# Performance work log

Measured on AMD Instinct MI355X. Metric: run time of the kernel, lower is better.

## Reference

```python
import jax, jax.numpy as jnp
import numpy as np

B, N, D, C, NCLS = 8, 2048, 256, 128, 50
EPS = 1e-5  # BatchNorm eps

def _bn(x, g, b):
    # eval-mode BatchNorm1d over channel dim of (B,C,N): running_mean=0, running_var=1
    return x * (g / jnp.sqrt(1.0 + EPS))[:, None] + b[:, None]

def _complex_linear(x, Wr, br, Wi, bi):
    # torch ComplexLinear: complex(fr(x.real)-fi(x.imag), fr(x.imag)+fi(x.real))
    xr, xi = x.real, x.imag
    re = (xr @ Wr.T + br) - (xi @ Wi.T + bi)
    im = (xi @ Wr.T + br) + (xr @ Wi.T + bi)
    return jax.lax.complex(re, im)

def _sa(x, qkW, vW, vb, tW, tb, g, b):
    # x: (B,C,N); q/k share weights (tied in torch), dim C//4
    xq = jnp.einsum('qc,bcn->bnq', qkW, x)            # (B,N,C/4)
    xk = jnp.einsum('qc,bcm->bqm', qkW, x)            # (B,C/4,N)
    energy = jnp.einsum('bnq,bqm->bnm', xq, xk)       # (B,N,N)
    attn = jax.nn.softmax(energy, axis=-1)
    attn = attn / (1e-9 + attn.sum(axis=1, keepdims=True))  # column renorm
    xv = jnp.einsum('oc,bcn->bon', vW, x) + vb[:, None]
    xr = x - jnp.einsum('bcn,bnm->bcm', xv, attn)
    xr = jnp.einsum('oc,bcn->bon', tW, xr) + tb[:, None]
    return x + jax.nn.relu(_bn(xr, g, b))

def reference(xyz, cls_label, A, Bmat, W1r, b1r, W1i, b1i, W2r, b2r, W2i, b2i,
              lbl_emb, ft_w1, ft_g1, ft_b1, ft_w2, ft_g2, ft_b2,
              sa_qk, sa_vw, sa_vb, sa_tw, sa_tb, sa_g, sa_b,
              fuse_w, fuse_g, fuse_b, c1_w, c1_b, bn1_g, bn1_b, c2_w, c2_b):
    pts = xyz.transpose(0, 2, 1)                       # (B,N,3)
    # VecKM(d=256, alpha=30, beta=9): G = eB (eB^H eA), normalized to sqrt(d)
    eA = jnp.exp(1j * (pts @ A))                       # (B,N,D) complex64
    eB = jnp.exp(1j * (pts @ Bmat))
    inner = jnp.einsum('bnd,bne->bde', eB.conj(), eA)  # (B,D,D)
    G = jnp.einsum('bnd,bde->bne', eB, inner)          # (B,N,D)
    G = G / jnp.linalg.norm(G, axis=-1, keepdims=True) * jnp.sqrt(jnp.float32(D))
    G = _complex_linear(G, W1r, b1r, W1i, b1i)
    G = jax.lax.complex(jax.nn.relu(G.real), jax.nn.relu(G.imag))  # ComplexReLU
    G = _complex_linear(G, W2r, b2r, W2i, b2i)
    G = (G.real ** 2 + G.imag ** 2).transpose(0, 2, 1)  # (B,D,N)
    reweight = (cls_label @ lbl_emb)[:, :, None]        # (B,D,1)
    x = G * reweight
    x = jax.nn.relu(_bn(jnp.einsum('oc,bcn->bon', ft_w1, x), ft_g1, ft_b1))
    x = _bn(jnp.einsum('oc,bcn->bon', ft_w2, x), ft_g2, ft_b2)  # (B,C,N)
    feats = []
    for i in range(4):
        x = _sa(x, sa_qk[i], sa_vw[i], sa_vb[i], sa_tw[i], sa_tb[i], sa_g[i], sa_b[i])
        feats.append(x)
    x = jnp.concatenate(feats, axis=1)                  # (B,4C,N)
    x = jax.nn.relu(_bn(jnp.einsum('oc,bcn->bon', fuse_w, x), fuse_g, fuse_b))
    x = jax.nn.relu(_bn(jnp.einsum('oc,bcn->bon', c1_w, x) + c1_b[:, None], bn1_g, bn1_b))
    # dropout is identity in eval mode
    x = jnp.einsum('oc,bcn->bon', c2_w, x) + c2_b[:, None]
    x = jax.nn.log_softmax(x, axis=1)
    return x.transpose(0, 2, 1)                         # (B,N,NCLS)

def setup_inputs():
    key = jax.random.key(0)
    k = jax.random.split(key, 24)
    rn = lambda i, s: jax.random.normal(k[i], s, jnp.float32)
    s = 0.05
    return {
        'xyz': rn(0, (B, 3, N)),
        'cls_label': jax.random.uniform(k[1], (B, 16), jnp.float32),
        'A': rn(2, (3, D)) * 30.0,
        'Bmat': rn(3, (3, D)) * 9.0,
        'W1r': rn(4, (D, D)) * s, 'b1r': rn(5, (D,)) * s,
        'W1i': rn(6, (D, D)) * s, 'b1i': rn(7, (D,)) * s,
        'W2r': rn(8, (D, D)) * s, 'b2r': rn(9, (D,)) * s,
        'W2i': rn(10, (D, D)) * s, 'b2i': rn(11, (D,)) * s,
        'lbl_emb': rn(12, (16, D)),
        'ft_w1': rn(13, (C, D)) * s, 'ft_g1': jnp.ones((C,)), 'ft_b1': jnp.zeros((C,)),
        'ft_w2': rn(14, (C, C)) * s, 'ft_g2': jnp.ones((C,)), 'ft_b2': jnp.zeros((C,)),
        'sa_qk': rn(15, (4, C // 4, C)) * s,
        'sa_vw': rn(16, (4, C, C)) * s, 'sa_vb': rn(17, (4, C)) * s,
        'sa_tw': rn(18, (4, C, C)) * s, 'sa_tb': rn(19, (4, C)) * s,
        'sa_g': jnp.ones((4, C)), 'sa_b': jnp.zeros((4, C)),
        'fuse_w': rn(20, (C, 4 * C)) * s, 'fuse_g': jnp.ones((C,)), 'fuse_b': jnp.zeros((C,)),
        'c1_w': rn(21, (C, C)) * s, 'c1_b': rn(22, (C,)) * s,
        'bn1_g': jnp.ones((C,)), 'bn1_b': jnp.zeros((C,)),
        'c2_w': rn(23, (NCLS, C)) * s, 'c2_b': jnp.zeros((NCLS,)),
    }
```

## Files before the change

### kernel.cpp

```cpp
#include <hip/hip_runtime.h>

#define BB 8
#define NPTS 2048
#define DD 256
#define CCH 128
#define NCLASS 50
#define LOG2E 1.4426950408889634f

typedef __attribute__((ext_vector_type(8))) short short8;
typedef __attribute__((ext_vector_type(4))) float f32x4;
typedef unsigned short u16;
#define MFMA16(a,b,c) __builtin_amdgcn_mfma_f32_16x16x32_bf16(a,b,c,0,0,0)

__device__ __forceinline__ u16 f2bf(float x){
  union { float f; unsigned int u; } v; v.f = x;
  unsigned int r = v.u + 0x7FFFu + ((v.u >> 16) & 1u);
  return (u16)(r >> 16);
}
__device__ __forceinline__ float bf2f(u16 u){
  union { unsigned int u32; float f; } v; v.u32 = ((unsigned int)u) << 16; return v.f;
}
__device__ __forceinline__ void split2(float x, u16& h, u16& l){
  h = f2bf(x); l = f2bf(x - bf2f(h));
}
__device__ __forceinline__ short8 ld8(const u16* p){ return *(const short8*)p; }
__device__ __forceinline__ short8 zero8(){ short8 z = {0,0,0,0,0,0,0,0}; return z; }

struct WSplit {
  const float* src[12];
  int cnt[12];
  int off[12];
};
__global__ __launch_bounds__(256) void wsplit_kernel(WSplit wsp, u16* __restrict__ H,
                                                     u16* __restrict__ L)
{
  int seg = blockIdx.y;
  int idx = blockIdx.x*256 + threadIdx.x;
  if (idx >= wsp.cnt[seg]) return;
  float v = wsp.src[seg][idx];
  u16 h, l; split2(v, h, l);
  H[wsp.off[seg]+idx] = h; L[wsp.off[seg]+idx] = l;
}

__global__ __launch_bounds__(256) void ek1_kernel(
    const float* __restrict__ xyz, const float* __restrict__ A, const float* __restrict__ Bm,
    u16* __restrict__ ATrh, u16* __restrict__ ATrl, u16* __restrict__ ATih, u16* __restrict__ ATil,
    u16* __restrict__ BTrh, u16* __restrict__ BTrl, u16* __restrict__ BTih, u16* __restrict__ BTil)
{
  size_t idx = (size_t)blockIdx.x*256 + threadIdx.x;
  int n = (int)(idx & (NPTS-1));
  int d = (int)((idx >> 11) & (DD-1));
  int b = (int)(idx >> 19);
  float p0 = xyz[((size_t)b*3+0)*NPTS+n];
  float p1 = xyz[((size_t)b*3+1)*NPTS+n];
  float p2 = xyz[((size_t)b*3+2)*NPTS+n];
  float phA = p0*A[d] + p1*A[DD+d] + p2*A[2*DD+d];
  float phB = p0*Bm[d] + p1*Bm[DD+d] + p2*Bm[2*DD+d];
  float sa, ca, sb, cb;
  sincosf(phA, &sa, &ca);
  sincosf(phB, &sb, &cb);
  size_t off = ((size_t)b*DD + d)*NPTS + n;
  u16 h, l;
  split2(ca, h, l); ATrh[off] = h; ATrl[off] = l;
  split2(sa, h, l); ATih[off] = h; ATil[off] = l;
  split2(cb, h, l); BTrh[off] = h; BTrl[off] = l;
  split2(sb, h, l); BTih[off] = h; BTil[off] = l;
}

__global__ __launch_bounds__(256) void ek2_kernel(
    const float* __restrict__ xyz, const float* __restrict__ Bm,
    u16* __restrict__ Brh, u16* __restrict__ Brl, u16* __restrict__ Bih, u16* __restrict__ Bil)
{
  size_t idx = (size_t)blockIdx.x*256 + threadIdx.x;
  int d = (int)(idx & (DD-1));
  int n = (int)((idx >> 8) & (NPTS-1));
  int b = (int)(idx >> 19);
  float p0 = xyz[((size_t)b*3+0)*NPTS+n];
  float p1 = xyz[((size_t)b*3+1)*NPTS+n];
  float p2 = xyz[((size_t)b*3+2)*NPTS+n];
  float phB = p0*Bm[d] + p1*Bm[DD+d] + p2*Bm[2*DD+d];
  float sb, cb;
  sincosf(phB, &sb, &cb);
  size_t off = ((size_t)b*NPTS + n)*DD + d;
  u16 h, l;
  split2(cb, h, l); Brh[off] = h; Brl[off] = l;
  split2(sb, h, l); Bih[off] = h; Bil[off] = l;
}

__global__ __launch_bounds__(256) void inner_mfma_kernel(
    const u16* __restrict__ ATrh, const u16* __restrict__ ATrl,
    const u16* __restrict__ ATih, const u16* __restrict__ ATil,
    const u16* __restrict__ BTrh, const u16* __restrict__ BTrl,
    const u16* __restrict__ BTih, const u16* __restrict__ BTil,
    float2* __restrict__ PART)
{
  int z = blockIdx.z; int b = z & 7; int ch = z >> 3;
  int e0 = blockIdx.y*64, d0 = blockIdx.x*64;
  int tid = threadIdx.x, lane = tid & 63, w = tid >> 6;
  int wr = (w >> 1)*32, wc = (w & 1)*32;
  int r16 = lane & 15, g4 = lane >> 4;
  f32x4 re[2][2] = {}, ip[2][2] = {}, iq[2][2] = {};
  size_t ar_[2], br_[2];
  #pragma unroll
  for (int rg = 0; rg < 2; rg++) {
    ar_[rg] = ((size_t)b*DD + (e0 + wr + rg*16 + r16))*NPTS + g4*8;
    br_[rg] = ((size_t)b*DD + (d0 + wc + rg*16 + r16))*NPTS + g4*8;
  }
  int kbeg = ch*512;
  #pragma unroll 2
  for (int kk = 0; kk < 512; kk += 32) {
    int k0 = kbeg + kk;
    short8 arh[2], arl[2], aih[2], ail[2], brh[2], brl[2], bih[2], bil[2];
    #pragma unroll
    for (int rg = 0; rg < 2; rg++) {
      arh[rg] = ld8(ATrh + ar_[rg] + k0); arl[rg] = ld8(ATrl + ar_[rg] + k0);
      aih[rg] = ld8(ATih + ar_[rg] + k0); ail[rg] = ld8(ATil + ar_[rg] + k0);
      brh[rg] = ld8(BTrh + br_[rg] + k0); brl[rg] = ld8(BTrl + br_[rg] + k0);
      bih[rg] = ld8(BTih + br_[rg] + k0); bil[rg] = ld8(BTil + br_[rg] + k0);
    }
    #pragma unroll
    for (int ra = 0; ra < 2; ra++)
      #pragma unroll
      for (int rb = 0; rb < 2; rb++) {
        re[ra][rb] = MFMA16(arh[ra], brh[rb], re[ra][rb]);
        re[ra][rb] = MFMA16(arh[ra], brl[rb], re[ra][rb]);
        re[ra][rb] = MFMA16(arl[ra], brh[rb], re[ra][rb]);
        re[ra][rb] = MFMA16(aih[ra], bih[rb], re[ra][rb]);
        re[ra][rb] = MFMA16(aih[ra], bil[rb], re[ra][rb]);
        re[ra][rb] = MFMA16(ail[ra], bih[rb], re[ra][rb]);
        ip[ra][rb] = MFMA16(aih[ra], brh[rb], ip[ra][rb]);
        ip[ra][rb] = MFMA16(aih[ra], brl[rb], ip[ra][rb]);
        ip[ra][rb] = MFMA16(ail[ra], brh[rb], ip[ra][rb]);
        iq[ra][rb] = MFMA16(arh[ra], bih[rb], iq[ra][rb]);
        iq[ra][rb] = MFMA16(arh[ra], bil[rb], iq[ra][rb]);
        iq[ra][rb] = MFMA16(arl[ra], bih[rb], iq[ra][rb]);
      }
  }
  float2* outp = PART + ((size_t)(ch*BB + b)*DD)*DD;
  #pragma unroll
  for (int ra = 0; ra < 2; ra++)
    #pragma unroll
    for (int rb = 0; rb < 2; rb++)
      #pragma unroll
      for (int j = 0; j < 4; j++) {
        int e = e0 + wr + ra*16 + g4*4 + j;
        int d = d0 + wc + rb*16 + r16;
        outp[(size_t)e*DD + d] = make_float2(re[ra][rb][j], ip[ra][rb][j] - iq[ra][rb][j]);
      }
}

__global__ __launch_bounds__(256) void innred_kernel(const float2* __restrict__ P,
    u16* __restrict__ Irh, u16* __restrict__ Irl, u16* __restrict__ Iih, u16* __restrict__ Iil)
{
  size_t i = (size_t)blockIdx.x*256 + threadIdx.x;
  const size_t S = (size_t)BB*DD*DD;
  float2 a = P[i], b = P[i+S], c = P[i+2*S], d = P[i+3*S];
  float rr = a.x+b.x+c.x+d.x, ii = a.y+b.y+c.y+d.y;
  u16 h, l;
  split2(rr, h, l); Irh[i] = h; Irl[i] = l;
  split2(ii, h, l); Iih[i] = h; Iil[i] = l;
}

__global__ __launch_bounds__(256) void g_mfma_kernel(
    const u16* __restrict__ Brh, const u16* __restrict__ Brl,
    const u16* __restrict__ Bih, const u16* __restrict__ Bil,
    const u16* __restrict__ Irh, const u16* __restrict__ Irl,
    const u16* __restrict__ Iih, const u16* __restrict__ Iil,
    float2* __restrict__ G)
{
  int b = blockIdx.z;
  int n0 = blockIdx.y*64, e0 = blockIdx.x*64;
  int tid = threadIdx.x, lane = tid & 63, w = tid >> 6;
  int wr = (w >> 1)*32, wc = (w & 1)*32;
  int r16 = lane & 15, g4 = lane >> 4;
  f32x4 p[2][2] = {}, q[2][2] = {}, im[2][2] = {};
  size_t ar_[2], br_[2];
  #pragma unroll
  for (int rg = 0; rg < 2; rg++) {
    ar_[rg] = ((size_t)b*NPTS + (n0 + wr + rg*16 + r16))*DD + g4*8;
    br_[rg] = ((size_t)b*DD + (e0 + wc + rg*16 + r16))*DD + g4*8;
  }
  #pragma unroll
  for (int k0 = 0; k0 < DD; k0 += 32) {
    short8 arh[2], arl[2], aih[2], ail[2], brh[2], brl[2], bih[2], bil[2];
    #pragma unroll
    for (int rg = 0; rg < 2; rg++) {
      arh[rg] = ld8(Brh + ar_[rg] + k0); arl[rg] = ld8(Brl + ar_[rg] + k0);
      aih[rg] = ld8(Bih + ar_[rg] + k0); ail[rg] = ld8(Bil + ar_[rg] + k0);
      brh[rg] = ld8(Irh + br_[rg] + k0); brl[rg] = ld8(Irl + br_[rg] + k0);
      bih[rg] = ld8(Iih + br_[rg] + k0); bil[rg] = ld8(Iil + br_[rg] + k0);
    }
    #pragma unroll
    for (int ra = 0; ra < 2; ra++)
      #pragma unroll
      for (int rb = 0; rb < 2; rb++) {
        p[ra][rb] = MFMA16(arh[ra], brh[rb], p[ra][rb]);
        p[ra][rb] = MFMA16(arh[ra], brl[rb], p[ra][rb]);
        p[ra][rb] = MFMA16(arl[ra], brh[rb], p[ra][rb]);
        q[ra][rb] = MFMA16(aih[ra], bih[rb], q[ra][rb]);
        q[ra][rb] = MFMA16(aih[ra], bil[rb], q[ra][rb]);
        q[ra][rb] = MFMA16(ail[ra], bih[rb], q[ra][rb]);
        im[ra][rb] = MFMA16(arh[ra], bih[rb], im[ra][rb]);
        im[ra][rb] = MFMA16(arh[ra], bil[rb], im[ra][rb]);
        im[ra][rb] = MFMA16(arl[ra], bih[rb], im[ra][rb]);
        im[ra][rb] = MFMA16(aih[ra], brh[rb], im[ra][rb]);
        im[ra][rb] = MFMA16(aih[ra], brl[rb], im[ra][rb]);
        im[ra][rb] = MFMA16(ail[ra], brh[rb], im[ra][rb]);
      }
  }
  #pragma unroll
  for (int ra = 0; ra < 2; ra++)
    #pragma unroll
    for (int rb = 0; rb < 2; rb++)
      #pragma unroll
      for (int j = 0; j < 4; j++) {
        int n = n0 + wr + ra*16 + g4*4 + j;
        int e = e0 + wc + rb*16 + r16;
        G[((size_t)b*NPTS + n)*DD + e] = make_float2(p[ra][rb][j] - q[ra][rb][j], im[ra][rb][j]);
      }
}

__global__ __launch_bounds__(256) void gnormsplit_kernel(const float2* __restrict__ Gf,
    u16* __restrict__ Grh, u16* __restrict__ Grl, u16* __restrict__ Gih, u16* __restrict__ Gil)
{
  size_t row = blockIdx.x;
  const float2* p = Gf + row*DD;
  int tid = threadIdx.x;
  float2 v = p[tid];
  __shared__ float red[256];
  red[tid] = v.x*v.x + v.y*v.y;
  __syncthreads();
  for (int w = 128; w > 0; w >>= 1) { if (tid < w) red[tid] += red[tid+w]; __syncthreads(); }
  float sc = 16.f * rsqrtf(red[0]);
  size_t off = row*DD + tid;
  u16 h, l;
  split2(v.x*sc, h, l); Grh[off] = h; Grl[off] = l;
  split2(v.y*sc, h, l); Gih[off] = h; Gil[off] = l;
}

__global__ __launch_bounds__(256) void clinear_mfma_kernel(
    const u16* __restrict__ Arh, const u16* __restrict__ Arl,
    const u16* __restrict__ Aih, const u16* __restrict__ Ail,
    const u16* __restrict__ Wrh, const u16* __restrict__ Wrl,
    const u16* __restrict__ Wih, const u16* __restrict__ Wil,
    const float* __restrict__ br, const float* __restrict__ bi,
    u16* __restrict__ Orh, u16* __restrict__ Orl, u16* __restrict__ Oih, u16* __restrict__ Oil,
    const float* __restrict__ RW, float* __restrict__ GSQ, int mode)
{
  int wg = blockIdx.y * gridDim.x + blockIdx.x;
  int xcd = wg & 7, idx = wg >> 3;
  int o0 = (idx & 3) * 64;
  int m0 = (xcd * ((int)gridDim.y >> 3) + (idx >> 2)) * 64;
  int tid = threadIdx.x, lane = tid & 63, w = tid >> 6;
  int wr = (w >> 1)*32, wc = (w & 1)*32;
  int r16 = lane & 15, g4 = lane >> 4;
  f32x4 p[2][2] = {}, q[2][2] = {}, im[2][2] = {};
  size_t ar_[2], br_[2];
  #pragma unroll
  for (int rg = 0; rg < 2; rg++) {
    ar_[rg] = (size_t)(m0 + wr + rg*16 + r16)*DD + g4*8;
    br_[rg] = (size_t)(o0 + wc + rg*16 + r16)*DD + g4*8;
  }
  #pragma unroll
  for (int k0 = 0; k0 < DD; k0 += 32) {
    short8 arh[2], arl[2], aih[2], ail[2], brh[2], brl[2], bih[2], bil[2];
    #pragma unroll
    for (int rg = 0; rg < 2; rg++) {
      arh[rg] = ld8(Arh + ar_[rg] + k0); arl[rg] = ld8(Arl + ar_[rg] + k0);
      aih[rg] = ld8(Aih + ar_[rg] + k0); ail[rg] = ld8(Ail + ar_[rg] + k0);
      brh[rg] = ld8(Wrh + br_[rg] + k0); brl[rg] = ld8(Wrl + br_[rg] + k0);
      bih[rg] = ld8(Wih + br_[rg] + k0); bil[rg] = ld8(Wil + br_[rg] + k0);
    }
    #pragma unroll
    for (int ra = 0; ra < 2; ra++)
      #pragma unroll
      for (int rb = 0; rb < 2; rb++) {
        p[ra][rb] = MFMA16(arh[ra], brh[rb], p[ra][rb]);
        p[ra][rb] = MFMA16(arh[ra], brl[rb], p[ra][rb]);
        p[ra][rb] = MFMA16(arl[ra], brh[rb], p[ra][rb]);
        q[ra][rb] = MFMA16(aih[ra], bih[rb], q[ra][rb]);
        q[ra][rb] = MFMA16(aih[ra], bil[rb], q[ra][rb]);
        q[ra][rb] = MFMA16(ail[ra], bih[rb], q[ra][rb]);
        im[ra][rb] = MFMA16(arh[ra], bih[rb], im[ra][rb]);
        im[ra][rb] = MFMA16(arh[ra], bil[rb], im[ra][rb]);
        im[ra][rb] = MFMA16(arl[ra], bih[rb], im[ra][rb]);
        im[ra][rb] = MFMA16(aih[ra], brh[rb], im[ra][rb]);
        im[ra][rb] = MFMA16(aih[ra], brl[rb], im[ra][rb]);
        im[ra][rb] = MFMA16(ail[ra], brh[rb], im[ra][rb]);
      }
  }
  #pragma unroll
  for (int ra = 0; ra < 2; ra++)
    #pragma unroll
    for (int rb = 0; rb < 2; rb++) {
      int o = o0 + wc + rb*16 + r16;
      float brv = br[o], biv = bi[o];
      if (mode == 1) {
        #pragma unroll
        for (int j = 0; j < 4; j++) {
          int m = m0 + wr + ra*16 + g4*4 + j;
          float re = fmaxf(p[ra][rb][j] - q[ra][rb][j] + brv - biv, 0.f);
          float iv = fmaxf(im[ra][rb][j] + brv + biv, 0.f);
          size_t off = (size_t)m*DD + o;
          u16 h, l;
          split2(re, h, l); Orh[off] = h; Orl[off] = l;
          split2(iv, h, l); Oih[off] = h; Oil[off] = l;
        }
      } else {
        int mbase = m0 + wr + ra*16 + g4*4;
        int b = mbase >> 11, nb = mbase & (NPTS-1);
        float rwv = RW[(size_t)b*DD + o];
        float4 gv;
        #pragma unroll
        for (int j = 0; j < 4; j++) {
          float re = p[ra][rb][j] - q[ra][rb][j] + brv - biv;
          float iv = im[ra][rb][j] + brv + biv;
          ((float*)&gv)[j] = (re*re + iv*iv) * rwv;
        }
        *(float4*)(GSQ + ((size_t)b*DD + o)*NPTS + nb) = gv;
      }
    }
}

__global__ void rw_kernel(const float* __restrict__ cls, const float* __restrict__ lbl,
                          float* __restrict__ RW)
{
  int b = blockIdx.x; int d = threadIdx.x;
  float s = 0.f;
  #pragma unroll
  for (int k = 0; k < 16; k++) s += cls[b*16+k] * lbl[k*DD+d];
  RW[b*DD+d] = s;
}

__global__ __launch_bounds__(256) void sgemm_kernel(
    const u16* __restrict__ Wh, const u16* __restrict__ Wl,
    const float* __restrict__ X, float* __restrict__ Y,
    const float* __restrict__ RES,
    const float* __restrict__ bias, const float* __restrict__ bng, const float* __restrict__ bnb,
    u16* __restrict__ YBh, u16* __restrict__ YBl, int ybmode,
    int O, int Cin, size_t xbs, size_t ybs, size_t rbs, int flags)
{
  int b = blockIdx.z;
  int n0 = blockIdx.x*64, o0 = blockIdx.y*64;
  const float* x = X + (size_t)b*xbs;
  __shared__ u16 sXh[64][40], sXl[64][40];
  int tid = threadIdx.x, lane = tid & 63, w = tid >> 6;
  int wo = (w >> 1)*32, wn = (w & 1)*32;
  int r16 = lane & 15, g4 = lane >> 4;
  f32x4 acc[2][2] = {};
  int stc = tid >> 3;
  int stn = (tid & 7)*8;
  for (int k0 = 0; k0 < Cin; k0 += 32) {
    const float* px = x + (size_t)(k0+stc)*NPTS + n0 + stn;
    float4 u0 = *(const float4*)px;
    float4 u1 = *(const float4*)(px+4);
    float v[8] = {u0.x,u0.y,u0.z,u0.w,u1.x,u1.y,u1.z,u1.w};
    __syncthreads();
    #pragma unroll
    for (int j = 0; j < 8; j++) {
      u16 h, l; split2(v[j], h, l);
      sXh[stn+j][stc] = h; sXl[stn+j][stc] = l;
    }
    __syncthreads();
    short8 awh[2], awl[2], bxh[2], bxl[2];
    #pragma unroll
    for (int rg = 0; rg < 2; rg++) {
      int orow = o0 + wo + rg*16 + r16;
      if (orow < O) {
        size_t woff = (size_t)orow*Cin + k0 + g4*8;
        awh[rg] = ld8(Wh + woff); awl[rg] = ld8(Wl + woff);
      } else { awh[rg] = zero8(); awl[rg] = zero8(); }
      bxh[rg] = ld8(&sXh[wn + rg*16 + r16][g4*8]);
      bxl[rg] = ld8(&sXl[wn + rg*16 + r16][g4*8]);
    }
    #pragma unroll
    for (int ra = 0; ra < 2; ra++)
      #pragma unroll
      for (int rb = 0; rb < 2; rb++) {
        acc[ra][rb] = MFMA16(awh[ra], bxh[rb], acc[ra][rb]);
        acc[ra][rb] = MFMA16(awh[ra], bxl[rb], acc[ra][rb]);
        acc[ra][rb] = MFMA16(awl[ra], bxh[rb], acc[ra][rb]);
      }
  }
  #pragma unroll
  for (int ra = 0; ra < 2; ra++)
    #pragma unroll
    for (int rb = 0; rb < 2; rb++)
      #pragma unroll
      for (int j = 0; j < 4; j++) {
        int o = o0 + wo + ra*16 + g4*4 + j;
        if (o >= O) continue;
        int n = n0 + wn + rb*16 + r16;
        float v = acc[ra][rb][j];
        if (flags & 1) v += bias[o];
        if (flags & 2) v = v * (bng[o] * rsqrtf(1.f + 1e-5f)) + bnb[o];
        if (flags & 4) v = fmaxf(v, 0.f);
        if (flags & 8) v += RES[(size_t)b*rbs + (size_t)o*NPTS + n];
        if (ybmode == 0) Y[(size_t)b*ybs + (size_t)o*NPTS + n] = v;
        else if (ybmode == 1) YBh[(size_t)b*ybs + (size_t)o*NPTS + n] = f2bf(v);
        else {
          u16 h, l; split2(v, h, l);
          size_t off = ((size_t)b*NPTS + n)*32 + o;
          YBh[off] = h; YBl[off] = l;
        }
      }
}

__global__ __launch_bounds__(256) void sastat_kernel(
    const u16* __restrict__ Qh, const u16* __restrict__ Ql,
    float* __restrict__ PM, float* __restrict__ PS)
{
  int b = blockIdx.z, ch = blockIdx.y;
  int n0 = blockIdx.x*64;
  size_t base = (size_t)b*NPTS*32;
  int tid = threadIdx.x, lane = tid & 63, wid = tid >> 6;
  int r16 = lane & 15, g4 = lane >> 4;
  size_t ao = base + (size_t)(n0 + wid*16 + r16)*32 + g4*8;
  short8 ah = ld8(Qh + ao), al = ld8(Ql + ao);
  float pm[4] = {-3.4e38f,-3.4e38f,-3.4e38f,-3.4e38f};
  float ps[4] = {0.f,0.f,0.f,0.f};
  int mbeg = ch*512, mend = mbeg + 512;
  for (int mt = mbeg; mt < mend; mt += 32) {
    size_t bo0 = base + (size_t)(mt + r16)*32 + g4*8;
    size_t bo1 = bo0 + 16*32;
    short8 bh0 = ld8(Qh+bo0), bl0 = ld8(Ql+bo0);
    short8 bh1 = ld8(Qh+bo1), bl1 = ld8(Ql+bo1);
    f32x4 a0 = {}, a1 = {};
    a0 = MFMA16(ah, bh0, a0); a0 = MFMA16(ah, bl0, a0); a0 = MFMA16(al, bh0, a0);
    a1 = MFMA16(ah, bh1, a1); a1 = MFMA16(ah, bl1, a1); a1 = MFMA16(al, bh1, a1);
    #pragma unroll
    for (int j = 0; j < 4; j++) {
      float v = fmaxf(a0[j], a1[j]);
      float mn = fmaxf(pm[j], v);
      ps[j] = ps[j]*exp2f((pm[j]-mn)*LOG2E)
            + exp2f((a0[j]-mn)*LOG2E) + exp2f((a1[j]-mn)*LOG2E);
      pm[j] = mn;
    }
  }
  #pragma unroll
  for (int j = 0; j < 4; j++) {
    float m = pm[j], s = ps[j];
    #pragma unroll
    for (int d = 1; d < 16; d <<= 1) {
      float om = __shfl_xor(m, d);
      float os = __shfl_xor(s, d);
      float mn = fmaxf(m, om);
      s = s*exp2f((m-mn)*LOG2E) + os*exp2f((om-mn)*LOG2E);
      m = mn;
    }
    if (r16 == 0) {
      int n_ = n0 + wid*16 + g4*4 + j;
      size_t off = ((size_t)ch*BB + b)*NPTS + n_;
      PM[off] = m; PS[off] = s;
    }
  }
}

__global__ __launch_bounds__(256) void comb1_kernel(
    const float* __restrict__ PM, const float* __restrict__ PS,
    float* __restrict__ MX, float* __restrict__ RS)
{
  size_t i = (size_t)blockIdx.x*256 + threadIdx.x;
  const size_t S = (size_t)BB*NPTS;
  float m0 = PM[i], m1 = PM[i+S], m2 = PM[i+2*S], m3 = PM[i+3*S];
  float mx = fmaxf(fmaxf(m0,m1), fmaxf(m2,m3));
  float den = PS[i]*exp2f((m0-mx)*LOG2E) + PS[i+S]*exp2f((m1-mx)*LOG2E)
            + PS[i+2*S]*exp2f((m2-mx)*LOG2E) + PS[i+3*S]*exp2f((m3-mx)*LOG2E);
  MX[i] = mx; RS[i] = 1.f/den;
}

__global__ __launch_bounds__(512) void fused_pv_kernel(
    const u16* __restrict__ Qh, const u16* __restrict__ Ql,
    const float* __restrict__ MX, const float* __restrict__ RS,
    const u16* __restrict__ XV, const float* __restrict__ XRES, size_t res_bs,
    float* __restrict__ OUT)
{
  int b = blockIdx.y;
  int m0 = blockIdx.x*64;
  size_t qbase = (size_t)b*NPTS*32;
  const u16* xv = XV + (size_t)b*CCH*NPTS;
  __shared__ float smx[NPTS], srs[NPTS];
  __shared__ u16 Pl[64][36];
  __shared__ float csacc[64];
  int tid = threadIdx.x, lane = tid & 63, w = tid >> 6;
  int r16 = lane & 15, g4 = lane >> 4;
  for (int t = tid; t < NPTS; t += 512) {
    smx[t] = MX[(size_t)b*NPTS + t];
    srs[t] = RS[(size_t)b*NPTS + t];
  }
  if (tid < 64) csacc[tid] = 0.f;
  int ma = w >> 1, na = w & 1;
  int cw = (w >> 1)*32, mw = (w & 1)*32;
  size_t eao = qbase + (size_t)(m0 + ma*16 + r16)*32 + g4*8;
  short8 eah = ld8(Qh + eao), eal = ld8(Ql + eao);
  const u16* pa0 = xv + (size_t)(cw + r16)*NPTS + g4*8;
  const u16* pa1 = pa0 + (size_t)16*NPTS;
  f32x4 acc[2][2] = {};
  float cs[4] = {0.f,0.f,0.f,0.f};
  size_t ebo = qbase + (size_t)(na*16 + r16)*32 + g4*8;
  short8 ebh = ld8(Qh + ebo), ebl = ld8(Ql + ebo);
  short8 xa0 = ld8(pa0), xa1 = ld8(pa1);
  __syncthreads();
  for (int nt = 0; nt < NPTS; nt += 32) {
    f32x4 e = {};
    e = MFMA16(eah, ebh, e); e = MFMA16(eah, ebl, e); e = MFMA16(eal, ebh, e);
    int nn = nt + na*16 + r16;
    float mxv_ = smx[nn], rsv_ = srs[nn];
    #pragma unroll
    for (int j = 0; j < 4; j++) {
      float t = exp2f((e[j]-mxv_)*LOG2E)*rsv_;
      cs[j] += t;
      Pl[ma*16 + g4*4 + j][na*16 + r16] = f2bf(t);
    }
    short8 nebh = zero8(), nebl = zero8(), nxa0 = zero8(), nxa1 = zero8();
    if (nt + 32 < NPTS) {
      size_t ebo2 = qbase + (size_t)(nt + 32 + na*16 + r16)*32 + g4*8;
      nebh = ld8(Qh + ebo2); nebl = ld8(Ql + ebo2);
      nxa0 = ld8(pa0 + nt + 32); nxa1 = ld8(pa1 + nt + 32);
    }
    __syncthreads();
    short8 b0 = *(const short8*)&Pl[mw + r16][g4*8];
    short8 b1 = *(const short8*)&Pl[mw + 16 + r16][g4*8];
    acc[0][0] = MFMA16(xa0, b0, acc[0][0]);
    acc[0][1] = MFMA16(xa0, b1, acc[0][1]);
    acc[1][0] = MFMA16(xa1, b0, acc[1][0]);
    acc[1][1] = MFMA16(xa1, b1, acc[1][1]);
    __syncthreads();
    ebh = nebh; ebl = nebl; xa0 = nxa0; xa1 = nxa1;
  }
  #pragma unroll
  for (int j = 0; j < 4; j++) {
    float c = cs[j];
    #pragma unroll
    for (int d = 1; d < 16; d <<= 1) c += __shfl_xor(c, d);
    if (r16 == 0) atomicAdd(&csacc[ma*16 + g4*4 + j], c);
  }
  __syncthreads();
  #pragma unroll
  for (int ca = 0; ca < 2; ca++)
    #pragma unroll
    for (int mb = 0; mb < 2; mb++) {
      int m = m0 + mw + mb*16 + r16;
      float ci = 1.f/(1e-9f + csacc[mw + mb*16 + r16]);
      #pragma unroll
      for (int j = 0; j < 4; j++) {
        int c = cw + ca*16 + g4*4 + j;
        float v = XRES[(size_t)b*res_bs + (size_t)c*NPTS + m] - acc[ca][mb][j]*ci;
        OUT[((size_t)b*CCH + c)*NPTS + m] = v;
      }
    }
}

__global__ __launch_bounds__(256) void lsm_kernel(const float* __restrict__ Y,
                                                  float* __restrict__ OUT)
{
  int idx = blockIdx.x*256 + threadIdx.x;
  int b = idx >> 11, n = idx & (NPTS-1);
  const float* p = Y + (size_t)b*NCLASS*NPTS + n;
  float m = -3.4e38f;
  #pragma unroll
  for (int k = 0; k < NCLASS; k++) m = fmaxf(m, p[(size_t)k*NPTS]);
  float s = 0.f;
  #pragma unroll
  for (int k = 0; k < NCLASS; k++) s += expf(p[(size_t)k*NPTS] - m);
  float L = m + logf(s);
  float* o = OUT + (size_t)idx*NCLASS;
  #pragma unroll
  for (int k = 0; k < NCLASS; k++) o[k] = p[(size_t)k*NPTS] - L;
}

extern "C" void kernel_launch(void* const* d_in, const int* in_sizes, int n_in,
                              void* d_out, int out_size, void* d_ws, size_t ws_size,
                              hipStream_t stream)
{
  (void)in_sizes; (void)n_in; (void)out_size; (void)ws_size;
  const float* xyz  = (const float*)d_in[0];
  const float* cls  = (const float*)d_in[1];
  const float* Amat = (const float*)d_in[2];
  const float* Bm   = (const float*)d_in[3];
  const float* W1r  = (const float*)d_in[4];
  const float* b1r  = (const float*)d_in[5];
  const float* W1i  = (const float*)d_in[6];
  const float* b1i  = (const float*)d_in[7];
  const float* W2r  = (const float*)d_in[8];
  const float* b2r  = (const float*)d_in[9];
  const float* W2i  = (const float*)d_in[10];
  const float* b2i  = (const float*)d_in[11];
  const float* lbl  = (const float*)d_in[12];
  const float* ftw1 = (const float*)d_in[13];
  const float* ftg1 = (const float*)d_in[14];
  const float* ftb1 = (const float*)d_in[15];
  const float* ftw2 = (const float*)d_in[16];
  const float* ftg2 = (const float*)d_in[17];
  const float* ftb2 = (const float*)d_in[18];
  const float* saqk = (const float*)d_in[19];
  const float* savw = (const float*)d_in[20];
  const float* savb = (const float*)d_in[21];
  const float* satw = (const float*)d_in[22];
  const float* satb = (const float*)d_in[23];
  const float* sag  = (const float*)d_in[24];
  const float* sab  = (const float*)d_in[25];
  const float* fusew= (const float*)d_in[26];
  const float* fuseg= (const float*)d_in[27];
  const float* fuseb= (const float*)d_in[28];
  const float* c1w  = (const float*)d_in[29];
  const float* c1b  = (const float*)d_in[30];
  const float* bn1g = (const float*)d_in[31];
  const float* bn1b = (const float*)d_in[32];
  const float* c2w  = (const float*)d_in[33];
  const float* c2b  = (const float*)d_in[34];
  float* out = (float*)d_out;

  float* ws = (float*)d_ws;
  const size_t PS  = (size_t)BB*DD*NPTS;
  const size_t ISZ = (size_t)BB*DD*DD;
  u16* U = (u16*)ws;
  u16 *ATrh = U+0*PS, *ATrl = U+1*PS, *ATih = U+2*PS, *ATil = U+3*PS;
  u16 *BTrh = U+4*PS, *BTrl = U+5*PS, *BTih = U+6*PS, *BTil = U+7*PS;
  u16 *Bnrh = U+8*PS, *Bnrl = U+9*PS, *Bnih = U+10*PS, *Bnil = U+11*PS;
  u16 *Irh = U+12*PS, *Irl = U+12*PS+ISZ, *Iih = U+12*PS+2*ISZ, *Iil = U+12*PS+3*ISZ;
  float* gsq = (float*)(U + 12*PS + 4*ISZ);
  float2* PART = (float2*)gsq;
  float2* Gf = (float2*)ws;
  u16 *G1rh = U+4*PS, *G1rl = U+5*PS, *G1ih = U+6*PS, *G1il = U+7*PS;
  u16 *G2rh = U+8*PS, *G2rl = U+9*PS, *G2ih = U+10*PS, *G2il = U+11*PS;
  size_t p = (size_t)BB*NPTS*NPTS;
  float* xfeat = ws + p;  p += (size_t)BB*CCH*NPTS;
  float* feats = ws + p;  p += (size_t)BB*4*CCH*NPTS;
  float* xt1   = ws + p;  p += (size_t)BB*CCH*NPTS;
  float* xt2   = ws + p;  p += (size_t)BB*CCH*NPTS;
  float* ybuf  = ws + p;  p += (size_t)BB*NCLASS*NPTS;
  float* rwb   = ws + p;  p += (size_t)BB*DD;
  float* mxv   = ws + p;  p += (size_t)BB*NPTS;
  float* rsv   = ws + p;  p += (size_t)BB*NPTS;
  float* PMb   = ws + p;  p += (size_t)4*BB*NPTS;
  float* PSb   = ws + p;  p += (size_t)4*BB*NPTS;
  u16* xqh = (u16*)(ws + p);
  u16* xql = xqh + (size_t)BB*NPTS*32;
  u16* xvb = xql + (size_t)BB*NPTS*32;
  u16* wpH = xvb + (size_t)BB*CCH*NPTS;
  u16* wpL = wpH + 557056;

  const int o_w1r=0, o_w1i=65536, o_w2r=131072, o_w2i=196608, o_ft1=262144,
            o_ft2=294912, o_qk=311296, o_vw=327680, o_tw=393216, o_fu=458752,
            o_c1=524288, o_c2=540672;
  WSplit wsp;
  const float* srcs[12] = {W1r,W1i,W2r,W2i,ftw1,ftw2,saqk,savw,satw,fusew,c1w,c2w};
  const int cnts[12] = {65536,65536,65536,65536,32768,16384,16384,65536,65536,65536,16384,6400};
  const int offs[12] = {o_w1r,o_w1i,o_w2r,o_w2i,o_ft1,o_ft2,o_qk,o_vw,o_tw,o_fu,o_c1,o_c2};
  for (int i = 0; i < 12; i++) { wsp.src[i]=srcs[i]; wsp.cnt[i]=cnts[i]; wsp.off[i]=offs[i]; }

  wsplit_kernel<<<dim3(256, 12), 256, 0, stream>>>(wsp, wpH, wpL);
  rw_kernel<<<BB, DD, 0, stream>>>(cls, lbl, rwb);
  ek1_kernel<<<(int)(PS/256), 256, 0, stream>>>(xyz, Amat, Bm,
      ATrh, ATrl, ATih, ATil, BTrh, BTrl, BTih, BTil);
  ek2_kernel<<<(int)(PS/256), 256, 0, stream>>>(xyz, Bm, Bnrh, Bnrl, Bnih, Bnil);
  inner_mfma_kernel<<<dim3(DD/64, DD/64, BB*4), 256, 0, stream>>>(
      ATrh, ATrl, ATih, ATil, BTrh, BTrl, BTih, BTil, PART);
  innred_kernel<<<(int)(ISZ/256), 256, 0, stream>>>(PART, Irh, Irl, Iih, Iil);
  g_mfma_kernel<<<dim3(DD/64, NPTS/64, BB), 256, 0, stream>>>(
      Bnrh, Bnrl, Bnih, Bnil, Irh, Irl, Iih, Iil, Gf);
  gnormsplit_kernel<<<BB*NPTS, 256, 0, stream>>>(Gf, G1rh, G1rl, G1ih, G1il);
  clinear_mfma_kernel<<<dim3(DD/64, (BB*NPTS)/64), 256, 0, stream>>>(
      G1rh, G1rl, G1ih, G1il, wpH+o_w1r, wpL+o_w1r, wpH+o_w1i, wpL+o_w1i,
      b1r, b1i, G2rh, G2rl, G2ih, G2il, nullptr, nullptr, 1);
  clinear_mfma_kernel<<<dim3(DD/64, (BB*NPTS)/64), 256, 0, stream>>>(
      G2rh, G2rl, G2ih, G2il, wpH+o_w2r, wpL+o_w2r, wpH+o_w2i, wpL+o_w2i,
      b2r, b2i, nullptr, nullptr, nullptr, nullptr, rwb, gsq, 2);

  sgemm_kernel<<<dim3(NPTS/64, CCH/64, BB), 256, 0, stream>>>(
      wpH+o_ft1, wpL+o_ft1, gsq, xt1, nullptr, nullptr, ftg1, ftb1, nullptr, nullptr, 0,
      CCH, DD, (size_t)DD*NPTS, (size_t)CCH*NPTS, 0, 2|4);
  sgemm_kernel<<<dim3(NPTS/64, CCH/64, BB), 256, 0, stream>>>(
      wpH+o_ft2, wpL+o_ft2, xt1, xfeat, nullptr, nullptr, ftg2, ftb2, nullptr, nullptr, 0,
      CCH, CCH, (size_t)CCH*NPTS, (size_t)CCH*NPTS, 0, 2);

  const float* xsrc = xfeat;
  size_t xbs = (size_t)CCH*NPTS;
  for (int i = 0; i < 4; i++) {
    sgemm_kernel<<<dim3(NPTS/64, 1, BB), 256, 0, stream>>>(
        wpH+o_qk + i*32*CCH, wpL+o_qk + i*32*CCH, xsrc, nullptr, nullptr,
        nullptr, nullptr, nullptr, xqh, xql, 2, 32, CCH, xbs, 0, 0, 0);
    sastat_kernel<<<dim3(NPTS/64, 4, BB), 256, 0, stream>>>(xqh, xql, PMb, PSb);
    comb1_kernel<<<(BB*NPTS)/256, 256, 0, stream>>>(PMb, PSb, mxv, rsv);
    sgemm_kernel<<<dim3(NPTS/64, CCH/64, BB), 256, 0, stream>>>(
        wpH+o_vw + i*CCH*CCH, wpL+o_vw + i*CCH*CCH, xsrc, nullptr, nullptr,
        savb + i*CCH, nullptr, nullptr, xvb, nullptr, 1, CCH, CCH, xbs,
        (size_t)CCH*NPTS, 0, 1);
    fused_pv_kernel<<<dim3(NPTS/64, BB), 512, 0, stream>>>(
        xqh, xql, mxv, rsv, xvb, xsrc, xbs, xt2);
    sgemm_kernel<<<dim3(NPTS/64, CCH/64, BB), 256, 0, stream>>>(
        wpH+o_tw + i*CCH*CCH, wpL+o_tw + i*CCH*CCH, xt2, feats + (size_t)i*CCH*NPTS, xsrc,
        satb + i*CCH, sag + i*CCH, sab + i*CCH, nullptr, nullptr, 0,
        CCH, CCH, (size_t)CCH*NPTS, (size_t)4*CCH*NPTS, xbs, 1|2|4|8);
    xsrc = feats + (size_t)i*CCH*NPTS;
    xbs = (size_t)4*CCH*NPTS;
  }

  sgemm_kernel<<<dim3(NPTS/64, CCH/64, BB), 256, 0, stream>>>(
      wpH+o_fu, wpL+o_fu, feats, xt1, nullptr, nullptr, fuseg, fuseb, nullptr, nullptr, 0,
      CCH, 4*CCH, (size_t)4*CCH*NPTS, (size_t)CCH*NPTS, 0, 2|4);
  sgemm_kernel<<<dim3(NPTS/64, CCH/64, BB), 256, 0, stream>>>(
      wpH+o_c1, wpL+o_c1, xt1, xt2, nullptr, c1b, bn1g, bn1b, nullptr, nullptr, 0,
      CCH, CCH, (size_t)CCH*NPTS, (size_t)CCH*NPTS, 0, 1|2|4);
  sgemm_kernel<<<dim3(NPTS/64, 1, BB), 256, 0, stream>>>(
      wpH+o_c2, wpL+o_c2, xt2, ybuf, nullptr, c2b, nullptr, nullptr, nullptr, nullptr, 0,
      NCLASS, CCH, (size_t)CCH*NPTS, (size_t)NCLASS*NPTS, 0, 1);
  lsm_kernel<<<(BB*NPTS)/256, 256, 0, stream>>>(ybuf, out);
}
```

Baseline: 970.5 us.

## Restructure fused attention-PV kernel to 16-column tiles with double-buffered P

Rewrites the fused softmax-times-V kernel so each 256-thread block handles 16 output columns instead of 64. Each wave computes a 16x16 chunk of attention probabilities for 64 keys per iteration into a double-buffered LDS tile, so one barrier per step is needed instead of two. Row max and inverse sum are read straight from global memory as float4 instead of being staged in LDS. The grid grows fourfold, which raises occupancy but recomputes more energy tiles per value load. The clinear kernel also drops its XCD-aware block swizzle in favour of a plain blockIdx mapping.

```diff
diff --git a/kernel.cpp b/kernel.cpp
--- a/kernel.cpp
+++ b/kernel.cpp
@@ -247,10 +247,7 @@
     u16* __restrict__ Orh, u16* __restrict__ Orl, u16* __restrict__ Oih, u16* __restrict__ Oil,
     const float* __restrict__ RW, float* __restrict__ GSQ, int mode)
 {
-  int wg = blockIdx.y * gridDim.x + blockIdx.x;
-  int xcd = wg & 7, idx = wg >> 3;
-  int o0 = (idx & 3) * 64;
-  int m0 = (xcd * ((int)gridDim.y >> 3) + (idx >> 2)) * 64;
+  int m0 = blockIdx.y*64, o0 = blockIdx.x*64;
   int tid = threadIdx.x, lane = tid & 63, w = tid >> 6;
   int wr = (w >> 1)*32, wc = (w & 1)*32;
   int r16 = lane & 15, g4 = lane >> 4;
@@ -469,85 +466,83 @@
   MX[i] = mx; RS[i] = 1.f/den;
 }
 
-__global__ __launch_bounds__(512) void fused_pv_kernel(
+__global__ __launch_bounds__(256) void fused_pv_kernel(
     const u16* __restrict__ Qh, const u16* __restrict__ Ql,
     const float* __restrict__ MX, const float* __restrict__ RS,
     const u16* __restrict__ XV, const float* __restrict__ XRES, size_t res_bs,
     float* __restrict__ OUT)
 {
   int b = blockIdx.y;
-  int m0 = blockIdx.x*64;
+  int m0 = blockIdx.x*16;
   size_t qbase = (size_t)b*NPTS*32;
   const u16* xv = XV + (size_t)b*CCH*NPTS;
-  __shared__ float smx[NPTS], srs[NPTS];
-  __shared__ u16 Pl[64][36];
-  __shared__ float csacc[64];
+  const float* mx = MX + (size_t)b*NPTS;
+  const float* rs = RS + (size_t)b*NPTS;
+  __shared__ u16 Pl[2][16][72];
+  __shared__ float csacc[16];
   int tid = threadIdx.x, lane = tid & 63, w = tid >> 6;
   int r16 = lane & 15, g4 = lane >> 4;
-  for (int t = tid; t < NPTS; t += 512) {
-    smx[t] = MX[(size_t)b*NPTS + t];
-    srs[t] = RS[(size_t)b*NPTS + t];
-  }
-  if (tid < 64) csacc[tid] = 0.f;
-  int ma = w >> 1, na = w & 1;
-  int cw = (w >> 1)*32, mw = (w & 1)*32;
-  size_t eao = qbase + (size_t)(m0 + ma*16 + r16)*32 + g4*8;
-  short8 eah = ld8(Qh + eao), eal = ld8(Ql + eao);
+  if (tid < 16) csacc[tid] = 0.f;
+  int nb = w;
+  int cw = w*32;
+  int nloc = nb*16 + g4*4;
+  size_t mo = qbase + (size_t)(m0 + r16)*32 + g4*8;
+  short8 mbh = ld8(Qh + mo), mbl = ld8(Ql + mo);
   const u16* pa0 = xv + (size_t)(cw + r16)*NPTS + g4*8;
   const u16* pa1 = pa0 + (size_t)16*NPTS;
-  f32x4 acc[2][2] = {};
-  float cs[4] = {0.f,0.f,0.f,0.f};
-  size_t ebo = qbase + (size_t)(na*16 + r16)*32 + g4*8;
-  short8 ebh = ld8(Qh + ebo), ebl = ld8(Ql + ebo);
-  short8 xa0 = ld8(pa0), xa1 = ld8(pa1);
+  f32x4 acc[2] = {};
+  float csl = 0.f;
+
+  #define COMPUTE_P(NT, BUF) { \
+    size_t no_ = qbase + (size_t)((NT) + nb*16 + r16)*32 + g4*8; \
+    short8 nah = ld8(Qh + no_), nal = ld8(Ql + no_); \
+    f32x4 e = {}; \
+    e = MFMA16(nah, mbh, e); e = MFMA16(nah, mbl, e); e = MFMA16(nal, mbh, e); \
+    float4 mx4 = *(const float4*)&mx[(NT) + nloc]; \
+    float4 rs4 = *(const float4*)&rs[(NT) + nloc]; \
+    float t0 = exp2f((e[0]-mx4.x)*LOG2E)*rs4.x; \
+    float t1 = exp2f((e[1]-mx4.y)*LOG2E)*rs4.y; \
+    float t2 = exp2f((e[2]-mx4.z)*LOG2E)*rs4.z; \
+    float t3 = exp2f((e[3]-mx4.w)*LOG2E)*rs4.w; \
+    csl += t0 + t1 + t2 + t3; \
+    uint2 pk; \
+    pk.x = (unsigned)f2bf(t0) | ((unsigned)f2bf(t1) << 16); \
+    pk.y = (unsigned)f2bf(t2) | ((unsigned)f2bf(t3) << 16); \
+    *(uint2*)&Pl[BUF][r16][nloc] = pk; }
+
+  COMPUTE_P(0, 0);
   __syncthreads();
-  for (int nt = 0; nt < NPTS; nt += 32) {
-    f32x4 e = {};
-    e = MFMA16(eah, ebh, e); e = MFMA16(eah, ebl, e); e = MFMA16(eal, ebh, e);
-    int nn = nt + na*16 + r16;
-    float mxv_ = smx[nn], rsv_ = srs[nn];
+  int cur = 0;
+  for (int nt = 0; nt < NPTS; nt += 64) {
+    short8 xa0 = ld8(pa0 + nt), xa1 = ld8(pa1 + nt);
+    short8 xb0 = ld8(pa0 + nt + 32), xb1 = ld8(pa1 + nt + 32);
+    short8 p0  = *(const short8*)&Pl[cur][r16][g4*8];
+    short8 p0b = *(const short8*)&Pl[cur][r16][32 + g4*8];
+    if (nt + 64 < NPTS) { COMPUTE_P(nt + 64, cur ^ 1); }
+    acc[0] = MFMA16(xa0, p0, acc[0]);
+    acc[1] = MFMA16(xa1, p0, acc[1]);
+    acc[0] = MFMA16(xb0, p0b, acc[0]);
+    acc[1] = MFMA16(xb1, p0b, acc[1]);
+    __syncthreads();
+    cur ^= 1;
+  }
+  #undef COMPUTE_P
+  {
+    float c = csl;
+    c += __shfl_xor(c, 16);
+    c += __shfl_xor(c, 32);
+    if (g4 == 0) atomicAdd(&csacc[r16], c);
+  }
+  __syncthreads();
+  float ci = 1.f/(1e-9f + csacc[r16]);
+  int m = m0 + r16;
+  #pragma unroll
+  for (int ca = 0; ca < 2; ca++)
     #pragma unroll
     for (int j = 0; j < 4; j++) {
-      float t = exp2f((e[j]-mxv_)*LOG2E)*rsv_;
-      cs[j] += t;
-      Pl[ma*16 + g4*4 + j][na*16 + r16] = f2bf(t);
-    }
-    short8 nebh = zero8(), nebl = zero8(), nxa0 = zero8(), nxa1 = zero8();
-    if (nt + 32 < NPTS) {
-      size_t ebo2 = qbase + (size_t)(nt + 32 + na*16 + r16)*32 + g4*8;
-      nebh = ld8(Qh + ebo2); nebl = ld8(Ql + ebo2);
-      nxa0 = ld8(pa0 + nt + 32); nxa1 = ld8(pa1 + nt + 32);
-    }
-    __syncthreads();
-    short8 b0 = *(const short8*)&Pl[mw + r16][g4*8];
-    short8 b1 = *(const short8*)&Pl[mw + 16 + r16][g4*8];
-    acc[0][0] = MFMA16(xa0, b0, acc[0][0]);
-    acc[0][1] = MFMA16(xa0, b1, acc[0][1]);
-    acc[1][0] = MFMA16(xa1, b0, acc[1][0]);
-    acc[1][1] = MFMA16(xa1, b1, acc[1][1]);
-    __syncthreads();
-    ebh = nebh; ebl = nebl; xa0 = nxa0; xa1 = nxa1;
-  }
-  #pragma unroll
-  for (int j = 0; j < 4; j++) {
-    float c = cs[j];
-    #pragma unroll
-    for (int d = 1; d < 16; d <<= 1) c += __shfl_xor(c, d);
-    if (r16 == 0) atomicAdd(&csacc[ma*16 + g4*4 + j], c);
-  }
-  __syncthreads();
-  #pragma unroll
-  for (int ca = 0; ca < 2; ca++)
-    #pragma unroll
-    for (int mb = 0; mb < 2; mb++) {
-      int m = m0 + mw + mb*16 + r16;
-      float ci = 1.f/(1e-9f + csacc[mw + mb*16 + r16]);
-      #pragma unroll
-      for (int j = 0; j < 4; j++) {
-        int c = cw + ca*16 + g4*4 + j;
-        float v = XRES[(size_t)b*res_bs + (size_t)c*NPTS + m] - acc[ca][mb][j]*ci;
-        OUT[((size_t)b*CCH + c)*NPTS + m] = v;
-      }
+      int c = cw + ca*16 + g4*4 + j;
+      float v = XRES[(size_t)b*res_bs + (size_t)c*NPTS + m] - acc[ca][j]*ci;
+      OUT[((size_t)b*CCH + c)*NPTS + m] = v;
     }
 }
 
@@ -687,7 +682,7 @@
         wpH+o_vw + i*CCH*CCH, wpL+o_vw + i*CCH*CCH, xsrc, nullptr, nullptr,
         savb + i*CCH, nullptr, nullptr, xvb, nullptr, 1, CCH, CCH, xbs,
         (size_t)CCH*NPTS, 0, 1);
-    fused_pv_kernel<<<dim3(NPTS/64, BB), 512, 0, stream>>>(
+    fused_pv_kernel<<<dim3(NPTS/16, BB), 256, 0, stream>>>(
         xqh, xql, mxv, rsv, xvb, xsrc, xbs, xt2);
     sgemm_kernel<<<dim3(NPTS/64, CCH/64, BB), 256, 0, stream>>>(
         wpH+o_tw + i*CCH*CCH, wpL+o_tw + i*CCH*CCH, xt2, feats + (size_t)i*CCH*NPTS, xsrc,
```

Result: slower. 997.1 us (+2.7%).
